# Optimization experiments

Hardware: AMD Instinct MI355X
Metric: run time of the kernel (lower is better)

## Reference

```python
import jax, jax.numpy as jnp
import numpy as np

N_CENTER, N_NEAR, N_STEPK, N_HOPS = 512, 32, 10, 2
FEAT_NAMES = ["xyz_fea", "pmt_fea", "mad_fea", "dim_fea", "nor_fea", "loc_fea", "fea"]


def pairwise_sqdist(x):
    # x: [B,N,C] -> [B,N,N]
    xx = jnp.sum(x * x, axis=-1)
    return xx[:, :, None] + xx[:, None, :] - 2.0 * jnp.einsum('bnc,bmc->bnm', x, x)


def surface_knn(x, n_near, n_stepk, n_hops=N_HOPS):
    # Iterative surface-KNN: build a step-KNN graph with n_stepk neighbors,
    # expand the neighborhood n_hops times (neighbor-of-neighbor union), then
    # pick the n_near nearest points among the reachable candidate set.
    d = pairwise_sqdist(x)                      # [B,N,N]
    B, N, _ = d.shape
    _, nbr = jax.lax.top_k(-d, n_stepk + 1)     # step neighbors (incl. self)
    b_idx = jnp.arange(B)[:, None, None]
    r_idx = jnp.arange(N)[None, :, None]
    adj = jnp.zeros((B, N, N), jnp.bool_).at[b_idx, r_idx, nbr].set(True)
    reach = adj
    adj_f = adj.astype(jnp.float32)
    for _ in range(n_hops):
        reach = (jnp.einsum('bij,bjk->bik', reach.astype(jnp.float32), adj_f) > 0) | adj
    dm = jnp.where(reach, d, jnp.inf)
    _, idx = jax.lax.top_k(-dm, n_near)         # [B,N,n_near], nearest reachable
    return idx


def fps(x, n_center):
    # Farthest point sampling in the C-dim feature space (dim=dim in source).
    B, N, _ = x.shape
    d = pairwise_sqdist(x)
    barange = jnp.arange(B)

    def step(carry, _):
        mind, prev = carry
        mind = jnp.minimum(mind, d[barange, prev])   # [B,N]
        nxt = jnp.argmax(mind, axis=-1).astype(jnp.int32)
        return (mind, nxt), nxt

    init = (jnp.full((B, N), jnp.inf, jnp.float32), jnp.zeros((B,), jnp.int32))
    _, rest = jax.lax.scan(step, init, None, length=n_center - 1)  # [S-1,B]
    idx = jnp.concatenate([jnp.zeros((1, B), jnp.int32), rest], axis=0)
    return idx.T                                   # [B,S]


def branch(center, grouped, wq, bq, wk, bk, wv, bv, w1, b1, w2, b2):
    # center: [B,S,C], grouped: [B,S,K,C]
    C = center.shape[-1]
    q = center @ wq + bq                           # [B,S,C]
    k = grouped @ wk + bk                          # [B,S,K,C]
    v = grouped @ wv + bv
    scores = jnp.einsum('bsc,bskc->bsk', q, k) / jnp.sqrt(jnp.float32(C))
    attn = jax.nn.softmax(scores, axis=-1)
    out = jnp.einsum('bsk,bskc->bsc', attn, v)     # attention pooling -> [B,S,C]
    h = jax.nn.relu(out @ w1 + b1)                 # MLP (C -> Cout -> Cout)
    return jax.nn.relu(h @ w2 + b2)


def setup_inputs() -> dict:
    key = jax.random.key(0)
    ks = jax.random.split(key, 16)
    B, N, C, CO = 8, 2048, 128, 256
    inp = {}
    for i, name in enumerate(FEAT_NAMES):
        inp[name] = jax.random.normal(ks[i], (B, N, C), jnp.float32)
    s = np.float32(1.0 / np.sqrt(C))
    so = np.float32(1.0 / np.sqrt(CO))
    inp['aw_q'] = jax.random.normal(ks[7], (7, C, C), jnp.float32) * s
    inp['ab_q'] = jnp.zeros((7, C), jnp.float32)
    inp['aw_k'] = jax.random.normal(ks[8], (7, C, C), jnp.float32) * s
    inp['ab_k'] = jnp.zeros((7, C), jnp.float32)
    inp['aw_v'] = jax.random.normal(ks[9], (7, C, C), jnp.float32) * s
    inp['ab_v'] = jnp.zeros((7, C), jnp.float32)
    inp['mw1'] = jax.random.normal(ks[10], (7, C, CO), jnp.float32) * s
    inp['mb1'] = jnp.zeros((7, CO), jnp.float32)
    inp['mw2'] = jax.random.normal(ks[11], (7, CO, CO), jnp.float32) * so
    inp['mb2'] = jnp.zeros((7, CO), jnp.float32)
    return inp


def reference(xyz_fea, pmt_fea, mad_fea, dim_fea, nor_fea, loc_fea, fea,
              aw_q, ab_q, aw_k, ab_k, aw_v, ab_v, mw1, mb1, mw2, mb2):
    B = xyz_fea.shape[0]
    feats = jnp.stack([xyz_fea, pmt_fea, mad_fea, dim_fea, nor_fea, loc_fea, fea], 0)  # [7,B,N,C]
    idx_all = surface_knn(xyz_fea, N_NEAR, N_STEPK)      # [B,N,K]
    fps_idx = fps(xyz_fea, N_CENTER)                     # [B,S]
    b2 = jnp.arange(B)[:, None]                          # [B,1]
    b3 = jnp.arange(B)[:, None, None]                    # [B,1,1]
    centers = feats[:, b2, fps_idx]                      # [7,B,S,C]
    idx = idx_all[b2, fps_idx]                           # [B,S,K]
    grouped = feats[:, b3, idx]                          # [7,B,S,K,C]
    outs = jax.vmap(branch)(centers, grouped, aw_q, ab_q, aw_k, ab_k,
                            aw_v, ab_v, mw1, mb1, mw2, mb2)  # [7,B,S,CO]
    return tuple(outs[i] for i in range(7))
```

## Files before the change

### kernel.cpp

```cpp
#include <hip/hip_runtime.h>
#include <hip/hip_bf16.h>
#include <math.h>

constexpr int BATCH = 8;
constexpr int NPTS  = 2048;
constexpr int CH    = 128;
constexpr int CHO   = 256;
constexpr int NCEN  = 512;
constexpr int NNEI  = 32;
constexpr int NTOP  = 11;
constexpr int NW    = 64;

struct Ptr7 { const float* p[7]; };

__global__ __launch_bounds__(256) void xx_kernel(const float* __restrict__ x,
                                                 float* __restrict__ xx) {
    int p = blockIdx.x * 256 + threadIdx.x;
    if (p >= BATCH * NPTS) return;
    const float4* xr = (const float4*)(x + (size_t)p * CH);
    float s = 0.f;
#pragma unroll
    for (int i = 0; i < CH / 4; i++) {
        float4 v = xr[i];
        s += v.x * v.x + v.y * v.y + v.z * v.z + v.w * v.w;
    }
    xx[p] = s;
}

__global__ __launch_bounds__(256) void dmat_kernel(const float* __restrict__ x,
                                                   const float* __restrict__ xx,
                                                   float* __restrict__ D) {
    __shared__ float As[32][68];
    __shared__ float Bs[32][68];
    int bz = blockIdx.z;
    int i0 = blockIdx.y * 64, j0 = blockIdx.x * 64;
    const float* X = x + (size_t)bz * NPTS * CH;
    int t = threadIdx.x, tx = t & 15, ty = t >> 4;
    int lr = t >> 3, lc = (t & 7) * 4;
    const float* ai0 = X + (size_t)(i0 + lr) * CH;
    const float* ai1 = X + (size_t)(i0 + lr + 32) * CH;
    const float* bj0 = X + (size_t)(j0 + lr) * CH;
    const float* bj1 = X + (size_t)(j0 + lr + 32) * CH;
    float acc[4][4] = {};
    for (int kc = 0; kc < CH; kc += 32) {
        float4 a0 = *(const float4*)(ai0 + kc + lc);
        float4 a1 = *(const float4*)(ai1 + kc + lc);
        float4 b0 = *(const float4*)(bj0 + kc + lc);
        float4 b1 = *(const float4*)(bj1 + kc + lc);
        __syncthreads();
        As[lc + 0][lr] = a0.x; As[lc + 1][lr] = a0.y; As[lc + 2][lr] = a0.z; As[lc + 3][lr] = a0.w;
        As[lc + 0][lr + 32] = a1.x; As[lc + 1][lr + 32] = a1.y; As[lc + 2][lr + 32] = a1.z; As[lc + 3][lr + 32] = a1.w;
        Bs[lc + 0][lr] = b0.x; Bs[lc + 1][lr] = b0.y; Bs[lc + 2][lr] = b0.z; Bs[lc + 3][lr] = b0.w;
        Bs[lc + 0][lr + 32] = b1.x; Bs[lc + 1][lr + 32] = b1.y; Bs[lc + 2][lr + 32] = b1.z; Bs[lc + 3][lr + 32] = b1.w;
        __syncthreads();
#pragma unroll
        for (int kk = 0; kk < 32; kk++) {
            float4 av = *(const float4*)&As[kk][ty * 4];
            float4 bv = *(const float4*)&Bs[kk][tx * 4];
            float a[4] = {av.x, av.y, av.z, av.w};
            float b[4] = {bv.x, bv.y, bv.z, bv.w};
#pragma unroll
            for (int i = 0; i < 4; i++)
#pragma unroll
                for (int j = 0; j < 4; j++) acc[i][j] += a[i] * b[j];
        }
    }
    const float* xxb = xx + bz * NPTS;
    float xi[4], xj[4];
#pragma unroll
    for (int i = 0; i < 4; i++) xi[i] = xxb[i0 + ty * 4 + i];
#pragma unroll
    for (int j = 0; j < 4; j++) xj[j] = xxb[j0 + tx * 4 + j];
#pragma unroll
    for (int i = 0; i < 4; i++) {
        float4 o;
        o.x = xi[i] + xj[0] - 2.f * acc[i][0];
        o.y = xi[i] + xj[1] - 2.f * acc[i][1];
        o.z = xi[i] + xj[2] - 2.f * acc[i][2];
        o.w = xi[i] + xj[3] - 2.f * acc[i][3];
        *(float4*)(D + ((size_t)bz * NPTS + i0 + ty * 4 + i) * NPTS + j0 + tx * 4) = o;
    }
}

__global__ __launch_bounds__(256) void knn_fps_kernel(const float* __restrict__ D,
                                                      unsigned int* __restrict__ adj,
                                                      int* __restrict__ fps_idx) {
    if (blockIdx.x < BATCH) {
        int lane = threadIdx.x;
        if (lane >= 64) return;
        int b = blockIdx.x;
        float mind[32];
#pragma unroll
        for (int r = 0; r < 32; r++) mind[r] = INFINITY;
        int prev = 0;
        if (lane == 0) fps_idx[b * NCEN] = 0;
        const float* Db = D + (size_t)b * NPTS * NPTS;
        for (int s = 1; s < NCEN; s++) {
            const float4* rowp = (const float4*)(Db + (size_t)prev * NPTS);
            float4 v0 = rowp[lane + 0 * 64];
            float4 v1 = rowp[lane + 1 * 64];
            float4 v2 = rowp[lane + 2 * 64];
            float4 v3 = rowp[lane + 3 * 64];
            float4 v4 = rowp[lane + 4 * 64];
            float4 v5 = rowp[lane + 5 * 64];
            float4 v6 = rowp[lane + 6 * 64];
            float4 v7 = rowp[lane + 7 * 64];
            float bv = -INFINITY; int bj = NPTS;
            float4 vv[8] = {v0, v1, v2, v3, v4, v5, v6, v7};
#pragma unroll
            for (int k = 0; k < 8; k++) {
                int j0 = 4 * (lane + 64 * k);
                float m0 = fminf(mind[4 * k + 0], vv[k].x); mind[4 * k + 0] = m0;
                float m1 = fminf(mind[4 * k + 1], vv[k].y); mind[4 * k + 1] = m1;
                float m2 = fminf(mind[4 * k + 2], vv[k].z); mind[4 * k + 2] = m2;
                float m3 = fminf(mind[4 * k + 3], vv[k].w); mind[4 * k + 3] = m3;
                if (m0 > bv) { bv = m0; bj = j0 + 0; }
                if (m1 > bv) { bv = m1; bj = j0 + 1; }
                if (m2 > bv) { bv = m2; bj = j0 + 2; }
                if (m3 > bv) { bv = m3; bj = j0 + 3; }
            }
#pragma unroll
            for (int off = 32; off > 0; off >>= 1) {
                float ov = __shfl_xor(bv, off);
                int oj = __shfl_xor(bj, off);
                if (ov > bv || (ov == bv && oj < bj)) { bv = ov; bj = oj; }
            }
            if (lane == 0) fps_idx[b * NCEN + s] = bj;
            prev = bj;
        }
        return;
    }
    __shared__ float row[NPTS];
    __shared__ float rv[256];
    __shared__ int ri[256];
    __shared__ int picks[NTOP + 1];
    int rid = blockIdx.x - BATCH;
    const float* Dr = D + (size_t)rid * NPTS;
    int t = threadIdx.x;
    float4* rp = (float4*)row;
    rp[t] = ((const float4*)Dr)[t];
    rp[t + 256] = ((const float4*)Dr)[t + 256];
    __syncthreads();
    for (int it = 0; it < NTOP; it++) {
        float bv = row[t];
        int bi = t;
#pragma unroll
        for (int k = 1; k < 8; k++) {
            int j = t + (k << 8);
            float v = row[j];
            if (v < bv) { bv = v; bi = j; }
        }
        rv[t] = bv; ri[t] = bi;
        __syncthreads();
        for (int off = 128; off > 0; off >>= 1) {
            if (t < off) {
                float ov = rv[t + off]; int oi = ri[t + off];
                if (ov < rv[t] || (ov == rv[t] && oi < ri[t])) { rv[t] = ov; ri[t] = oi; }
            }
            __syncthreads();
        }
        if (t == 0) { picks[it] = ri[0]; row[ri[0]] = INFINITY; }
        __syncthreads();
    }
    if (t < NW) {
        unsigned w = 0;
#pragma unroll
        for (int p = 0; p < NTOP; p++) {
            int j = picks[p];
            if ((j >> 5) == t) w |= 1u << (j & 31);
        }
        adj[(size_t)rid * NW + t] = w;
    }
}

__global__ void make_gather(const int* __restrict__ fps_idx, int* __restrict__ gatherC) {
    int r = blockIdx.x * 256 + threadIdx.x;
    if (r >= BATCH * NCEN) return;
    int b = r >> 9, s = r & 511;
    gatherC[r] = b * NPTS + fps_idx[b * NCEN + s];
}

__global__ __launch_bounds__(256) void reach_top32_kernel(const unsigned int* __restrict__ adj,
                                                          const float* __restrict__ D,
                                                          const int* __restrict__ fps_idx,
                                                          int* __restrict__ idx_sel) {
    __shared__ unsigned adjw[NW], R1[NW], R2[NW];
    __shared__ int lst[NPTS];
    __shared__ float dst[NPTS];
    __shared__ int cnt;
    __shared__ float rv[256];
    __shared__ int rj[256], rp[256];
    __shared__ int sel[NNEI];
    int s = blockIdx.x, b = blockIdx.y, t = threadIdx.x;
    int i = fps_idx[b * NCEN + s];
    const unsigned* arow = adj + ((size_t)(b * NPTS + i)) * NW;
    if (t < NW) { adjw[t] = arow[t]; R1[t] = arow[t]; }
    if (t == 0) cnt = 0;
    __syncthreads();
    if (t < NW) {
        unsigned w = adjw[t];
        while (w) { int bb = __ffs(w) - 1; w &= w - 1; int p = atomicAdd(&cnt, 1); lst[p] = t * 32 + bb; }
    }
    __syncthreads();
    int n1 = cnt;
    {
        int g = t >> 6, lane = t & 63;
        for (int p = g; p < n1; p += 4) {
            unsigned aw = adj[((size_t)(b * NPTS + lst[p])) * NW + lane];
            atomicOr(&R1[lane], aw);
        }
    }
    __syncthreads();
    if (t == 0) cnt = 0;
    __syncthreads();
    if (t < NW) {
        unsigned w = R1[t];
        while (w) { int bb = __ffs(w) - 1; w &= w - 1; int p = atomicAdd(&cnt, 1); lst[p] = t * 32 + bb; }
        R2[t] = adjw[t];
    }
    __syncthreads();
    int n2 = cnt;
    {
        int g = t >> 6, lane = t & 63;
        for (int p = g; p < n2; p += 4) {
            unsigned aw = adj[((size_t)(b * NPTS + lst[p])) * NW + lane];
            atomicOr(&R2[lane], aw);
        }
    }
    __syncthreads();
    if (t == 0) cnt = 0;
    __syncthreads();
    const float* Dr = D + (size_t)(b * NPTS + i) * NPTS;
    if (t < NW) {
        unsigned w = R2[t];
        while (w) {
            int bb = __ffs(w) - 1; w &= w - 1;
            int j = t * 32 + bb;
            int p = atomicAdd(&cnt, 1);
            lst[p] = j; dst[p] = Dr[j];
        }
    }
    __syncthreads();
    int L = cnt;
    int nsel = L < NNEI ? L : NNEI;
    for (int r = 0; r < nsel; r++) {
        float bv = INFINITY; int bj = 0x7fffffff, bp = -1;
        for (int p = t; p < L; p += 256) {
            float v = dst[p]; int j = lst[p];
            if (v < bv || (v == bv && j < bj)) { bv = v; bj = j; bp = p; }
        }
        rv[t] = bv; rj[t] = bj; rp[t] = bp;
        __syncthreads();
        for (int off = 128; off > 0; off >>= 1) {
            if (t < off) {
                if (rv[t + off] < rv[t] || (rv[t + off] == rv[t] && rj[t + off] < rj[t])) {
                    rv[t] = rv[t + off]; rj[t] = rj[t + off]; rp[t] = rp[t + off];
                }
            }
            __syncthreads();
        }
        if (t == 0) { sel[r] = rj[0]; dst[rp[0]] = INFINITY; }
        __syncthreads();
    }
    if (t == 0 && nsel < NNEI) {
        int r = nsel;
        for (int j = 0; j < NPTS && r < NNEI; j++)
            if (!((R2[j >> 5] >> (j & 31)) & 1)) sel[r++] = j;
    }
    __syncthreads();
    if (t < NNEI) idx_sel[((size_t)(b * NCEN + s)) * NNEI + t] = sel[t];
}

template <int KSIZE, bool RELU>
__device__ __forceinline__ void gemm_tile64(const float* __restrict__ A, int lda,
                                            const int* __restrict__ gather,
                                            const float* __restrict__ W, int ldw,
                                            const float* __restrict__ bias,
                                            float* __restrict__ Out, int ldo) {
    __shared__ float As[32][68];
    __shared__ float Ws[32][68];
    int t = threadIdx.x;
    int tx = t & 15, ty = t >> 4;
    int lr = t >> 3, lc = (t & 7) * 4;
    const float* ar0 = A + (size_t)(gather ? gather[lr] : lr) * lda;
    const float* ar1 = A + (size_t)(gather ? gather[lr + 32] : lr + 32) * lda;
    float acc[4][4] = {};
    for (int kc = 0; kc < KSIZE; kc += 32) {
        float4 a0 = *(const float4*)(ar0 + kc + lc);
        float4 a1 = *(const float4*)(ar1 + kc + lc);
        float4 w0 = *(const float4*)(W + (size_t)(kc + lr) * ldw + lc);
        float4 w1 = *(const float4*)(W + (size_t)(kc + lr) * ldw + lc + 32);
        __syncthreads();
        As[lc + 0][lr] = a0.x; As[lc + 1][lr] = a0.y; As[lc + 2][lr] = a0.z; As[lc + 3][lr] = a0.w;
        As[lc + 0][lr + 32] = a1.x; As[lc + 1][lr + 32] = a1.y; As[lc + 2][lr + 32] = a1.z; As[lc + 3][lr + 32] = a1.w;
        *(float4*)&Ws[lr][lc] = w0;
        *(float4*)&Ws[lr][lc + 32] = w1;
        __syncthreads();
#pragma unroll
        for (int kk = 0; kk < 32; kk++) {
            float4 av = *(const float4*)&As[kk][ty * 4];
            float4 wv = *(const float4*)&Ws[kk][tx * 4];
            float a[4] = {av.x, av.y, av.z, av.w};
            float w[4] = {wv.x, wv.y, wv.z, wv.w};
#pragma unroll
            for (int i = 0; i < 4; i++)
#pragma unroll
                for (int j = 0; j < 4; j++) acc[i][j] += a[i] * w[j];
        }
    }
#pragma unroll
    for (int i = 0; i < 4; i++) {
        int r = ty * 4 + i;
        float4 o;
        o.x = acc[i][0] + bias[tx * 4 + 0];
        o.y = acc[i][1] + bias[tx * 4 + 1];
        o.z = acc[i][2] + bias[tx * 4 + 2];
        o.w = acc[i][3] + bias[tx * 4 + 3];
        if (RELU) {
            o.x = fmaxf(o.x, 0.f); o.y = fmaxf(o.y, 0.f);
            o.z = fmaxf(o.z, 0.f); o.w = fmaxf(o.w, 0.f);
        }
        *(float4*)(Out + (size_t)r * ldo + tx * 4) = o;
    }
}

__global__ __launch_bounds__(256) void kvproj_kernel(Ptr7 feats, const float* __restrict__ awk,
                                                     const float* __restrict__ abk,
                                                     const float* __restrict__ awv,
                                                     const float* __restrict__ abv,
                                                     float* __restrict__ ktab,
                                                     float* __restrict__ vtab) {
    int v = blockIdx.z, ct = blockIdx.y, rt = blockIdx.x;
    bool isv = ct >= 2;
    int c2 = ct & 1;
    const float* A = feats.p[v] + (size_t)rt * 64 * CH;
    const float* W = (isv ? awv : awk) + (size_t)v * CH * CH + c2 * 64;
    const float* bias = (isv ? abv : abk) + v * CH + c2 * 64;
    float* Out = (isv ? vtab : ktab) + (size_t)v * (BATCH * NPTS) * CH + (size_t)rt * 64 * CH + c2 * 64;
    gemm_tile64<CH, false>(A, CH, nullptr, W, CH, bias, Out, CH);
}

__global__ __launch_bounds__(256) void qproj_kernel(Ptr7 feats, const float* __restrict__ awq,
                                                    const float* __restrict__ abq,
                                                    const int* __restrict__ gatherC,
                                                    float* __restrict__ qtab) {
    int v = blockIdx.z, ct = blockIdx.y, rt = blockIdx.x;
    gemm_tile64<CH, false>(feats.p[v], CH, gatherC + rt * 64,
                           awq + (size_t)v * CH * CH + ct * 64, CH,
                           abq + v * CH + ct * 64,
                           qtab + ((size_t)v * (BATCH * NCEN) + rt * 64) * CH + ct * 64, CH);
}

__global__ __launch_bounds__(256) void mlp1_kernel(const float* __restrict__ otab,
                                                   const float* __restrict__ mw1,
                                                   const float* __restrict__ mb1,
                                                   float* __restrict__ htab) {
    int v = blockIdx.z, ct = blockIdx.y, rt = blockIdx.x;
    gemm_tile64<CH, true>(otab + ((size_t)v * (BATCH * NCEN) + rt * 64) * CH, CH, nullptr,
                          mw1 + (size_t)v * CH * CHO + ct * 64, CHO,
                          mb1 + v * CHO + ct * 64,
                          htab + ((size_t)v * (BATCH * NCEN) + rt * 64) * CHO + ct * 64, CHO);
}

__global__ __launch_bounds__(256) void mlp2_kernel(const float* __restrict__ htab,
                                                   const float* __restrict__ mw2,
                                                   const float* __restrict__ mb2,
                                                   float* __restrict__ out) {
    int v = blockIdx.z, ct = blockIdx.y, rt = blockIdx.x;
    gemm_tile64<CHO, true>(htab + ((size_t)v * (BATCH * NCEN) + rt * 64) * CHO, CHO, nullptr,
                           mw2 + (size_t)v * CHO * CHO + ct * 64, CHO,
                           mb2 + v * CHO + ct * 64,
                           out + ((size_t)v * (BATCH * NCEN) + rt * 64) * CHO + ct * 64, CHO);
}

__global__ __launch_bounds__(256) void attn_kernel(const float* __restrict__ qtab,
                                                   const float* __restrict__ ktab,
                                                   const float* __restrict__ vtab,
                                                   const int* __restrict__ idx_sel,
                                                   float* __restrict__ otab) {
    __shared__ float q_s[4][CH];
    __shared__ float attn_s[4][NNEI];
    __shared__ int jj_s[4][NNEI];
    int v = blockIdx.y;
    int t = threadIdx.x, w = t >> 6, lane = t & 63;
    int cg = blockIdx.x * 4 + w;
    int b = cg >> 9, s = cg & 511;
    const float* qr = qtab + ((size_t)v * (BATCH * NCEN) + cg) * CH;
    *(float2*)&q_s[w][lane * 2] = *(const float2*)(qr + lane * 2);
    if (lane < NNEI) jj_s[w][lane] = idx_sel[((size_t)(b * NCEN + s)) * NNEI + lane];
    __syncthreads();
    if (lane < NNEI) {
        int j = jj_s[w][lane];
        const float* kr = ktab + ((size_t)v * (BATCH * NPTS) + b * NPTS + j) * CH;
        float acc = 0.f;
#pragma unroll
        for (int c4 = 0; c4 < CH / 4; c4++) {
            float4 qv = *(const float4*)&q_s[w][c4 * 4];
            float4 kv = *(const float4*)(kr + c4 * 4);
            acc += qv.x * kv.x + qv.y * kv.y + qv.z * kv.z + qv.w * kv.w;
        }
        float sc = acc * 0.08838834764831845f;
        float m = sc;
#pragma unroll
        for (int off = 16; off > 0; off >>= 1) m = fmaxf(m, __shfl_xor(m, off, 32));
        float e = expf(sc - m);
        float sum = e;
#pragma unroll
        for (int off = 16; off > 0; off >>= 1) sum += __shfl_xor(sum, off, 32);
        attn_s[w][lane] = e / sum;
    }
    __syncthreads();
    float2 o = {0.f, 0.f};
    const float* vbase = vtab + ((size_t)v * (BATCH * NPTS) + b * NPTS) * CH;
    for (int tt = 0; tt < NNEI; tt++) {
        int j = jj_s[w][tt];
        float a = attn_s[w][tt];
        float2 vv = *(const float2*)(vbase + (size_t)j * CH + lane * 2);
        o.x += a * vv.x;
        o.y += a * vv.y;
    }
    *(float2*)(otab + ((size_t)v * (BATCH * NCEN) + cg) * CH + lane * 2) = o;
}

extern "C" void kernel_launch(void* const* d_in, const int* in_sizes, int n_in,
                              void* d_out, int out_size, void* d_ws, size_t ws_size,
                              hipStream_t stream) {
    (void)in_sizes; (void)n_in; (void)out_size;
    Ptr7 feats;
    for (int i = 0; i < 7; i++) feats.p[i] = (const float*)d_in[i];
    const float* awq = (const float*)d_in[7];
    const float* abq = (const float*)d_in[8];
    const float* awk = (const float*)d_in[9];
    const float* abk = (const float*)d_in[10];
    const float* awv = (const float*)d_in[11];
    const float* abv = (const float*)d_in[12];
    const float* mw1 = (const float*)d_in[13];
    const float* mb1 = (const float*)d_in[14];
    const float* mw2 = (const float*)d_in[15];
    const float* mb2 = (const float*)d_in[16];
    const float* xyz = feats.p[0];

    char* ws = (char*)d_ws;
    size_t SZ_D = (size_t)BATCH * NPTS * NPTS * 4;
    float* D = (float*)ws;
    float* ktab = (float*)ws;
    float* vtab = (float*)(ws + (size_t)7 * BATCH * NPTS * CH * 4);
    size_t off = SZ_D;
    float* xx = (float*)(ws + off); off += (size_t)BATCH * NPTS * 4;
    unsigned* adjb = (unsigned*)(ws + off); off += (size_t)BATCH * NPTS * NW * 4;
    int* fpsidx = (int*)(ws + off); off += (size_t)BATCH * NCEN * 4;
    int* idxsel = (int*)(ws + off); off += (size_t)BATCH * NCEN * NNEI * 4;
    int* gatherC = (int*)(ws + off); off += (size_t)BATCH * NCEN * 4;
    float* qtab = (float*)(ws + off); off += (size_t)7 * BATCH * NCEN * CH * 4;
    float* otab = (float*)(ws + off); off += (size_t)7 * BATCH * NCEN * CH * 4;
    float* htab = (float*)(ws + off); off += (size_t)7 * BATCH * NCEN * CHO * 4;
    if (ws_size < off) return;

    xx_kernel<<<dim3((BATCH * NPTS + 255) / 256), dim3(256), 0, stream>>>(xyz, xx);
    dmat_kernel<<<dim3(NPTS / 64, NPTS / 64, BATCH), dim3(256), 0, stream>>>(xyz, xx, D);
    knn_fps_kernel<<<dim3(BATCH + BATCH * NPTS), dim3(256), 0, stream>>>(D, adjb, fpsidx);
    make_gather<<<dim3((BATCH * NCEN + 255) / 256), dim3(256), 0, stream>>>(fpsidx, gatherC);
    reach_top32_kernel<<<dim3(NCEN, BATCH), dim3(256), 0, stream>>>(adjb, D, fpsidx, idxsel);
    kvproj_kernel<<<dim3(BATCH * NPTS / 64, 4, 7), dim3(256), 0, stream>>>(feats, awk, abk, awv, abv, ktab, vtab);
    qproj_kernel<<<dim3(BATCH * NCEN / 64, 2, 7), dim3(256), 0, stream>>>(feats, awq, abq, gatherC, qtab);
    attn_kernel<<<dim3(BATCH * NCEN / 4, 7), dim3(256), 0, stream>>>(qtab, ktab, vtab, idxsel, otab);
    mlp1_kernel<<<dim3(BATCH * NCEN / 64, 4, 7), dim3(256), 0, stream>>>(otab, mw1, mb1, htab);
    mlp2_kernel<<<dim3(BATCH * NCEN / 64, 4, 7), dim3(256), 0, stream>>>(htab, mw2, mb2, (float*)d_out);
}
```

Measured before the change: 1.162 ms.

## Exploit distance symmetry, stage FPS rows through LDS, unify shared memory buffers

The distance-matrix kernel now computes only upper-triangle tiles and writes each off-diagonal tile twice, once directly and once transposed through shared memory. This halves the GEMM work at the cost of an extra shared-memory transpose, and half the blocks exit immediately. The FPS loop in the renamed front kernel loads each row with global_load_lds into LDS. It replaces the shuffle-based argmax with a serial scan of 64 candidates from LDS done by every lane. Shared memory in all GEMM kernels is moved to a single raw byte buffer, mainly as cleanup.

```diff
diff --git a/kernel.cpp b/kernel.cpp
--- a/kernel.cpp
+++ b/kernel.cpp
@@ -10,6 +10,7 @@
 constexpr int NNEI  = 32;
 constexpr int NTOP  = 11;
 constexpr int NW    = 64;
+constexpr int SMEM_BYTES = 17408;
 
 struct Ptr7 { const float* p[7]; };
 
@@ -30,10 +31,13 @@
 __global__ __launch_bounds__(256) void dmat_kernel(const float* __restrict__ x,
                                                    const float* __restrict__ xx,
                                                    float* __restrict__ D) {
-    __shared__ float As[32][68];
-    __shared__ float Bs[32][68];
+    __shared__ __align__(16) char smem[SMEM_BYTES];
+    int it = blockIdx.y, jt = blockIdx.x;
+    if (jt < it) return;
+    float (*As)[68] = (float(*)[68])smem;
+    float (*Bs)[68] = (float(*)[68])(smem + 32 * 68 * 4);
     int bz = blockIdx.z;
-    int i0 = blockIdx.y * 64, j0 = blockIdx.x * 64;
+    int i0 = it * 64, j0 = jt * 64;
     const float* X = x + (size_t)bz * NPTS * CH;
     int t = threadIdx.x, tx = t & 15, ty = t >> 4;
     int lr = t >> 3, lc = (t & 7) * 4;
@@ -71,24 +75,46 @@
     for (int i = 0; i < 4; i++) xi[i] = xxb[i0 + ty * 4 + i];
 #pragma unroll
     for (int j = 0; j < 4; j++) xj[j] = xxb[j0 + tx * 4 + j];
+    float ov[4][4];
+#pragma unroll
+    for (int i = 0; i < 4; i++)
+#pragma unroll
+        for (int j = 0; j < 4; j++) ov[i][j] = xi[i] + xj[j] - 2.f * acc[i][j];
 #pragma unroll
     for (int i = 0; i < 4; i++) {
-        float4 o;
-        o.x = xi[i] + xj[0] - 2.f * acc[i][0];
-        o.y = xi[i] + xj[1] - 2.f * acc[i][1];
-        o.z = xi[i] + xj[2] - 2.f * acc[i][2];
-        o.w = xi[i] + xj[3] - 2.f * acc[i][3];
+        float4 o = {ov[i][0], ov[i][1], ov[i][2], ov[i][3]};
         *(float4*)(D + ((size_t)bz * NPTS + i0 + ty * 4 + i) * NPTS + j0 + tx * 4) = o;
     }
-}
-
-__global__ __launch_bounds__(256) void knn_fps_kernel(const float* __restrict__ D,
-                                                      unsigned int* __restrict__ adj,
-                                                      int* __restrict__ fps_idx) {
+    if (jt > it) {
+        __syncthreads();
+        float (*T)[65] = (float(*)[65])smem;
+#pragma unroll
+        for (int i = 0; i < 4; i++)
+#pragma unroll
+            for (int j = 0; j < 4; j++) T[ty * 4 + i][tx * 4 + j] = ov[i][j];
+        __syncthreads();
+#pragma unroll
+        for (int i = 0; i < 4; i++) {
+            float4 o;
+            o.x = T[tx * 4 + 0][ty * 4 + i];
+            o.y = T[tx * 4 + 1][ty * 4 + i];
+            o.z = T[tx * 4 + 2][ty * 4 + i];
+            o.w = T[tx * 4 + 3][ty * 4 + i];
+            *(float4*)(D + ((size_t)bz * NPTS + j0 + ty * 4 + i) * NPTS + i0 + tx * 4) = o;
+        }
+    }
+}
+
+__global__ __launch_bounds__(256) void fused_front_kernel(const float* __restrict__ D,
+                                                          unsigned int* __restrict__ adj,
+                                                          int* __restrict__ fps_idx) {
+    __shared__ __align__(16) char smem[SMEM_BYTES];
     if (blockIdx.x < BATCH) {
         int lane = threadIdx.x;
         if (lane >= 64) return;
         int b = blockIdx.x;
+        float* row_lds = (float*)smem;
+        float2* red = (float2*)(smem + 8192);
         float mind[32];
 #pragma unroll
         for (int r = 0; r < 32; r++) mind[r] = INFINITY;
@@ -96,44 +122,55 @@
         if (lane == 0) fps_idx[b * NCEN] = 0;
         const float* Db = D + (size_t)b * NPTS * NPTS;
         for (int s = 1; s < NCEN; s++) {
-            const float4* rowp = (const float4*)(Db + (size_t)prev * NPTS);
-            float4 v0 = rowp[lane + 0 * 64];
-            float4 v1 = rowp[lane + 1 * 64];
-            float4 v2 = rowp[lane + 2 * 64];
-            float4 v3 = rowp[lane + 3 * 64];
-            float4 v4 = rowp[lane + 4 * 64];
-            float4 v5 = rowp[lane + 5 * 64];
-            float4 v6 = rowp[lane + 6 * 64];
-            float4 v7 = rowp[lane + 7 * 64];
+            const float* rowg = Db + (size_t)prev * NPTS;
+#pragma unroll
+            for (int k = 0; k < 8; k++) {
+                __builtin_amdgcn_global_load_lds(
+                    (const __attribute__((address_space(1))) unsigned int*)(rowg + 4 * (lane + 64 * k)),
+                    (__attribute__((address_space(3))) unsigned int*)(row_lds + 256 * k),
+                    16, 0, 0);
+            }
+            asm volatile("s_waitcnt vmcnt(0)" ::: "memory");
             float bv = -INFINITY; int bj = NPTS;
-            float4 vv[8] = {v0, v1, v2, v3, v4, v5, v6, v7};
 #pragma unroll
             for (int k = 0; k < 8; k++) {
+                float4 g = ((const float4*)row_lds)[lane + 64 * k];
                 int j0 = 4 * (lane + 64 * k);
-                float m0 = fminf(mind[4 * k + 0], vv[k].x); mind[4 * k + 0] = m0;
-                float m1 = fminf(mind[4 * k + 1], vv[k].y); mind[4 * k + 1] = m1;
-                float m2 = fminf(mind[4 * k + 2], vv[k].z); mind[4 * k + 2] = m2;
-                float m3 = fminf(mind[4 * k + 3], vv[k].w); mind[4 * k + 3] = m3;
+                float m0 = fminf(mind[4 * k + 0], g.x); mind[4 * k + 0] = m0;
+                float m1 = fminf(mind[4 * k + 1], g.y); mind[4 * k + 1] = m1;
+                float m2 = fminf(mind[4 * k + 2], g.z); mind[4 * k + 2] = m2;
+                float m3 = fminf(mind[4 * k + 3], g.w); mind[4 * k + 3] = m3;
                 if (m0 > bv) { bv = m0; bj = j0 + 0; }
                 if (m1 > bv) { bv = m1; bj = j0 + 1; }
                 if (m2 > bv) { bv = m2; bj = j0 + 2; }
                 if (m3 > bv) { bv = m3; bj = j0 + 3; }
             }
-#pragma unroll
-            for (int off = 32; off > 0; off >>= 1) {
-                float ov = __shfl_xor(bv, off);
-                int oj = __shfl_xor(bj, off);
-                if (ov > bv || (ov == bv && oj < bj)) { bv = ov; bj = oj; }
+            red[lane] = make_float2(bv, __int_as_float(bj));
+            float cv[4]; int cj[4];
+#pragma unroll
+            for (int c = 0; c < 4; c++) {
+                float v = -INFINITY; int j = NPTS;
+#pragma unroll
+                for (int k = 0; k < 16; k++) {
+                    float2 e = red[c * 16 + k];
+                    int ej = __float_as_int(e.y);
+                    if (e.x > v || (e.x == v && ej < j)) { v = e.x; j = ej; }
+                }
+                cv[c] = v; cj[c] = j;
             }
-            if (lane == 0) fps_idx[b * NCEN + s] = bj;
-            prev = bj;
+            float bestv = cv[0]; int bestj = cj[0];
+#pragma unroll
+            for (int c = 1; c < 4; c++)
+                if (cv[c] > bestv || (cv[c] == bestv && cj[c] < bestj)) { bestv = cv[c]; bestj = cj[c]; }
+            if (lane == 0) fps_idx[b * NCEN + s] = bestj;
+            prev = bestj;
         }
         return;
     }
-    __shared__ float row[NPTS];
-    __shared__ float rv[256];
-    __shared__ int ri[256];
-    __shared__ int picks[NTOP + 1];
+    float* row = (float*)smem;
+    float* rv = row + NPTS;
+    int* ri = (int*)(rv + 256);
+    int* picks = ri + 256;
     int rid = blockIdx.x - BATCH;
     const float* Dr = D + (size_t)rid * NPTS;
     int t = threadIdx.x;
@@ -154,8 +191,8 @@
         __syncthreads();
         for (int off = 128; off > 0; off >>= 1) {
             if (t < off) {
-                float ov = rv[t + off]; int oi = ri[t + off];
-                if (ov < rv[t] || (ov == rv[t] && oi < ri[t])) { rv[t] = ov; ri[t] = oi; }
+                float ovv = rv[t + off]; int oi = ri[t + off];
+                if (ovv < rv[t] || (ovv == rv[t] && oi < ri[t])) { rv[t] = ovv; ri[t] = oi; }
             }
             __syncthreads();
         }
@@ -272,13 +309,14 @@
 }
 
 template <int KSIZE, bool RELU>
-__device__ __forceinline__ void gemm_tile64(const float* __restrict__ A, int lda,
+__device__ __forceinline__ void gemm_tile64(char* smem,
+                                            const float* __restrict__ A, int lda,
                                             const int* __restrict__ gather,
                                             const float* __restrict__ W, int ldw,
                                             const float* __restrict__ bias,
                                             float* __restrict__ Out, int ldo) {
-    __shared__ float As[32][68];
-    __shared__ float Ws[32][68];
+    float (*As)[68] = (float(*)[68])smem;
+    float (*Ws)[68] = (float(*)[68])(smem + 32 * 68 * 4);
     int t = threadIdx.x;
     int tx = t & 15, ty = t >> 4;
     int lr = t >> 3, lc = (t & 7) * 4;
@@ -330,6 +368,7 @@
                                                      const float* __restrict__ abv,
                                                      float* __restrict__ ktab,
                                                      float* __restrict__ vtab) {
+    __shared__ __align__(16) char smem[SMEM_BYTES];
     int v = blockIdx.z, ct = blockIdx.y, rt = blockIdx.x;
     bool isv = ct >= 2;
     int c2 = ct & 1;
@@ -337,15 +376,16 @@
     const float* W = (isv ? awv : awk) + (size_t)v * CH * CH + c2 * 64;
     const float* bias = (isv ? abv : abk) + v * CH + c2 * 64;
     float* Out = (isv ? vtab : ktab) + (size_t)v * (BATCH * NPTS) * CH + (size_t)rt * 64 * CH + c2 * 64;
-    gemm_tile64<CH, false>(A, CH, nullptr, W, CH, bias, Out, CH);
+    gemm_tile64<CH, false>(smem, A, CH, nullptr, W, CH, bias, Out, CH);
 }
 
 __global__ __launch_bounds__(256) void qproj_kernel(Ptr7 feats, const float* __restrict__ awq,
                                                     const float* __restrict__ abq,
                                                     const int* __restrict__ gatherC,
                                                     float* __restrict__ qtab) {
+    __shared__ __align__(16) char smem[SMEM_BYTES];
     int v = blockIdx.z, ct = blockIdx.y, rt = blockIdx.x;
-    gemm_tile64<CH, false>(feats.p[v], CH, gatherC + rt * 64,
+    gemm_tile64<CH, false>(smem, feats.p[v], CH, gatherC + rt * 64,
                            awq + (size_t)v * CH * CH + ct * 64, CH,
                            abq + v * CH + ct * 64,
                            qtab + ((size_t)v * (BATCH * NCEN) + rt * 64) * CH + ct * 64, CH);
@@ -355,8 +395,9 @@
                                                    const float* __restrict__ mw1,
                                                    const float* __restrict__ mb1,
                                                    float* __restrict__ htab) {
+    __shared__ __align__(16) char smem[SMEM_BYTES];
     int v = blockIdx.z, ct = blockIdx.y, rt = blockIdx.x;
-    gemm_tile64<CH, true>(otab + ((size_t)v * (BATCH * NCEN) + rt * 64) * CH, CH, nullptr,
+    gemm_tile64<CH, true>(smem, otab + ((size_t)v * (BATCH * NCEN) + rt * 64) * CH, CH, nullptr,
                           mw1 + (size_t)v * CH * CHO + ct * 64, CHO,
                           mb1 + v * CHO + ct * 64,
                           htab + ((size_t)v * (BATCH * NCEN) + rt * 64) * CHO + ct * 64, CHO);
@@ -366,8 +407,9 @@
                                                    const float* __restrict__ mw2,
                                                    const float* __restrict__ mb2,
                                                    float* __restrict__ out) {
+    __shared__ __align__(16) char smem[SMEM_BYTES];
     int v = blockIdx.z, ct = blockIdx.y, rt = blockIdx.x;
-    gemm_tile64<CHO, true>(htab + ((size_t)v * (BATCH * NCEN) + rt * 64) * CHO, CHO, nullptr,
+    gemm_tile64<CHO, true>(smem, htab + ((size_t)v * (BATCH * NCEN) + rt * 64) * CHO, CHO, nullptr,
                            mw2 + (size_t)v * CHO * CHO + ct * 64, CHO,
                            mb2 + v * CHO + ct * 64,
                            out + ((size_t)v * (BATCH * NCEN) + rt * 64) * CHO + ct * 64, CHO);
@@ -458,7 +500,7 @@
 
     xx_kernel<<<dim3((BATCH * NPTS + 255) / 256), dim3(256), 0, stream>>>(xyz, xx);
     dmat_kernel<<<dim3(NPTS / 64, NPTS / 64, BATCH), dim3(256), 0, stream>>>(xyz, xx, D);
-    knn_fps_kernel<<<dim3(BATCH + BATCH * NPTS), dim3(256), 0, stream>>>(D, adjb, fpsidx);
+    fused_front_kernel<<<dim3(BATCH + BATCH * NPTS), dim3(256), 0, stream>>>(D, adjb, fpsidx);
     make_gather<<<dim3((BATCH * NCEN + 255) / 256), dim3(256), 0, stream>>>(fpsidx, gatherC);
     reach_top32_kernel<<<dim3(NCEN, BATCH), dim3(256), 0, stream>>>(adjb, D, fpsidx, idxsel);
     kvproj_kernel<<<dim3(BATCH * NPTS / 64, 4, 7), dim3(256), 0, stream>>>(feats, awk, abk, awv, abv, ktab, vtab);
```

New measurement: 3.144 ms. 2.71x slower.
